# Kernel tuning notes

Hardware: AMD Instinct MI355X
Metric: run time of the kernel (lower is better)

## Reference

```python
import jax, jax.numpy as jnp
import numpy as np

EMB_DIM = 1024
NUM_HEADS = 16
HEAD_DIM = EMB_DIM // NUM_HEADS


def setup_inputs() -> dict:
    key = jax.random.key(0)
    ks = jax.random.split(key, 10)
    B, Sq, Skv = 4, 4096, 4096
    scale = 1.0 / np.sqrt(EMB_DIM)
    inp = {
        "query": jax.random.normal(ks[0], (B, Sq, EMB_DIM), jnp.float32),
        "key_value": jax.random.normal(ks[1], (B, Skv, EMB_DIM), jnp.float32),
        "Wq": jax.random.normal(ks[2], (EMB_DIM, EMB_DIM), jnp.float32) * scale,
        "bq": jnp.zeros((EMB_DIM,), jnp.float32),
        "Wk": jax.random.normal(ks[3], (EMB_DIM, EMB_DIM), jnp.float32) * scale,
        "bk": jnp.zeros((EMB_DIM,), jnp.float32),
        "Wv": jax.random.normal(ks[4], (EMB_DIM, EMB_DIM), jnp.float32) * scale,
        "bv": jnp.zeros((EMB_DIM,), jnp.float32),
        "Wo": jax.random.normal(ks[5], (EMB_DIM, EMB_DIM), jnp.float32) * scale,
        "bo": jnp.zeros((EMB_DIM,), jnp.float32),
    }
    return inp


def reference(query, key_value, Wq, bq, Wk, bk, Wv, bv, Wo, bo):
    B, Sq, D = query.shape
    Skv = key_value.shape[1]
    H, hd = NUM_HEADS, HEAD_DIM
    # Projections -> [B, S, H, hd]
    Q = (query @ Wq + bq).reshape(B, Sq, H, hd)
    K = (key_value @ Wk + bk).reshape(B, Skv, H, hd)
    V = (key_value @ Wv + bv).reshape(B, Skv, H, hd)
    # elu+1 feature map (strictly positive)
    Q = jax.nn.elu(Q) + 1.0
    K = jax.nn.elu(K) + 1.0
    # KV summarization: [B, H, hd, hd]
    KV = jnp.einsum("bshd,bshe->bhde", K, V)
    K_sum = K.sum(axis=1)  # [B, H, hd]
    # Attention output and normalizer
    out = jnp.einsum("bqhd,bhde->bqhe", Q, KV)          # [B, Sq, H, hd]
    norm = jnp.einsum("bqhd,bhd->bqh", Q, K_sum)         # [B, Sq, H]
    out = out / (norm[..., None] + 1e-6)
    out = out.reshape(B, Sq, D)
    return out @ Wo + bo  # dropout is identity in eval
```

## Files before the change

kernel.cpp:

```cpp
#include <hip/hip_runtime.h>

typedef __bf16 bf16_t;
typedef __bf16 bf16x2 __attribute__((ext_vector_type(2)));
typedef __bf16 bf16x8 __attribute__((ext_vector_type(8)));
typedef float floatx4 __attribute__((ext_vector_type(4)));

#define B_ 4
#define S_ 4096
#define D_ 1024
#define H_ 16
#define HD_ 64
#define M_TOT (B_ * S_)

#define BM 128
#define BN 128
#define BK 64

__device__ __forceinline__ void async_load16(const bf16_t* g, bf16_t* l) {
  __builtin_amdgcn_global_load_lds(
      (const __attribute__((address_space(1))) void*)g,
      (__attribute__((address_space(3))) void*)l,
      16, 0, 0);
}

struct PrepArgs {
  const float* q; const float* kv;
  bf16_t* aq; bf16_t* akv;
  const float* w0; const float* w1; const float* w2; const float* w3;
  bf16_t* t0; bf16_t* t1; bf16_t* t2; bf16_t* t3;
  float* zbase;
};

__global__ __launch_bounds__(256) void prep_kernel(PrepArgs p) {
  __shared__ float tile[32][33];
  const int bid = blockIdx.x;
  const int t = threadIdx.x;
  if (bid < 16384) {
    const float* in = bid < 8192 ? p.q : p.kv;
    bf16_t* out = bid < 8192 ? p.aq : p.akv;
    int i = ((bid & 8191) * 256 + t) * 8;
    float4 a = *(const float4*)(in + i);
    float4 b = *(const float4*)(in + i + 4);
    bf16x8 o;
    o[0] = (bf16_t)a.x; o[1] = (bf16_t)a.y; o[2] = (bf16_t)a.z; o[3] = (bf16_t)a.w;
    o[4] = (bf16_t)b.x; o[5] = (bf16_t)b.y; o[6] = (bf16_t)b.z; o[7] = (bf16_t)b.w;
    *(bf16x8*)(out + i) = o;
  } else if (bid < 20480) {
    int idx = bid - 16384;
    int z = idx >> 10;
    int rem = idx & 1023;
    const float* W = z == 0 ? p.w0 : z == 1 ? p.w1 : z == 2 ? p.w2 : p.w3;
    bf16_t* Wt = z == 0 ? p.t0 : z == 1 ? p.t1 : z == 2 ? p.t2 : p.t3;
    int n0 = (rem & 31) * 32;
    int k0 = (rem >> 5) * 32;
    int tx = t & 31;
    int ty = t >> 5;
    for (int r = ty; r < 32; r += 8)
      tile[r][tx] = W[(size_t)(k0 + r) * D_ + n0 + tx];
    __syncthreads();
    for (int r = ty; r < 32; r += 8)
      Wt[(size_t)(n0 + r) * D_ + k0 + tx] = (bf16_t)tile[tx][r];
  } else {
    int idx = bid - 20480;
    ((float4*)p.zbase)[idx * 256 + t] = (float4){0.f, 0.f, 0.f, 0.f};
  }
}

struct ProjArgs {
  const bf16_t* Aq; const bf16_t* Akv;
  const bf16_t* WqT; const bf16_t* WkvT;
  const float* bq; const float* bk; const float* bv;
  bf16_t* Qf; bf16_t* Kf; bf16_t* Vf;
};

__global__ __launch_bounds__(256) void proj_kernel(ProjArgs p) {
  __shared__ __attribute__((aligned(16))) bf16_t As[BM * BK];
  __shared__ __attribute__((aligned(16))) bf16_t Bs[BN * BK];
  const int t = threadIdx.x;
  const int w = t >> 6;
  const int lane = t & 63;

  const unsigned L = blockIdx.x;
  const unsigned xcd = L & 7;
  const unsigned slot = L >> 3;
  const unsigned mt = xcd * 16 + slot / 24u;
  const unsigned nt = slot % 24u;
  const int row0 = mt * BM;
  const bool isQ = nt < 8;
  const bf16_t* A  = isQ ? p.Aq : p.Akv;
  const bf16_t* Bt = isQ ? p.WqT : p.WkvT;
  const int col0 = (isQ ? nt : nt - 8) * BN;

  const int wm = (w & 1) * 64;
  const int wn = (w >> 1) * 64;
  const int lr = lane & 15;
  const int lq = lane >> 4;
  const int rx = lr & 7;

  floatx4 acc[4][4];
#pragma unroll
  for (int i = 0; i < 4; ++i)
#pragma unroll
    for (int j = 0; j < 4; ++j) acc[i][j] = (floatx4){0.f, 0.f, 0.f, 0.f};

  for (int kt = 0; kt < D_; kt += BK) {
#pragma unroll
    for (int j = 0; j < 4; ++j) {
      int s = j * 256 + t;
      int r = s >> 3;
      int cs = (((s & 7) ^ (r & 7)) << 3);
      async_load16(&A[(size_t)(row0 + r) * D_ + kt + cs], &As[j * 2048 + w * 512]);
      async_load16(&Bt[(size_t)(col0 + r) * D_ + kt + cs], &Bs[j * 2048 + w * 512]);
    }
    __syncthreads();
#pragma unroll
    for (int ks = 0; ks < BK; ks += 32) {
      const int go = ((lq + (ks >> 3)) ^ rx) << 3;
      bf16x8 af[4], bfr[4];
#pragma unroll
      for (int i = 0; i < 4; ++i)
        af[i] = *(const bf16x8*)&As[(wm + i * 16 + lr) * BK + go];
#pragma unroll
      for (int j = 0; j < 4; ++j)
        bfr[j] = *(const bf16x8*)&Bs[(wn + j * 16 + lr) * BK + go];
#pragma unroll
      for (int i = 0; i < 4; ++i)
#pragma unroll
        for (int j = 0; j < 4; ++j)
          acc[i][j] = __builtin_amdgcn_mfma_f32_16x16x32_bf16(af[i], bfr[j], acc[i][j], 0, 0, 0);
    }
    __syncthreads();
  }

#pragma unroll
  for (int i = 0; i < 4; ++i) {
#pragma unroll
    for (int j = 0; j < 4; ++j) {
      int gr = row0 + wm + i * 16 + lq * 4;
      int gc = col0 + wn + j * 16 + lr;
      if (isQ) {
        float bsv = p.bq[gc];
#pragma unroll
        for (int r = 0; r < 4; ++r) {
          float v = acc[i][j][r] + bsv;
          v = v > 0.f ? v + 1.f : __expf(v);
          p.Qf[(size_t)(gr + r) * 1024 + gc] = (bf16_t)v;
        }
      } else if (gc < 1024) {
        float bsv = p.bk[gc];
#pragma unroll
        for (int r = 0; r < 4; ++r) {
          float v = acc[i][j][r] + bsv;
          v = v > 0.f ? v + 1.f : __expf(v);
          p.Kf[(size_t)(gr + r) * 1024 + gc] = (bf16_t)v;
        }
      } else {
        float bsv = p.bv[gc - 1024];
#pragma unroll
        for (int r = 0; r < 4; ++r) {
          float v = acc[i][j][r] + bsv;
          p.Vf[(size_t)(gr + r) * 1024 + (gc - 1024)] = (bf16_t)v;
        }
      }
    }
  }
}

__global__ __launch_bounds__(256) void gemm_out_kernel(
    const bf16_t* __restrict__ A,
    const bf16_t* __restrict__ Bt,
    const float* __restrict__ bias,
    float* __restrict__ outf) {
  __shared__ __attribute__((aligned(16))) bf16_t As[BM * BK];
  __shared__ __attribute__((aligned(16))) bf16_t Bs[BN * BK];
  const int t = threadIdx.x;
  const int w = t >> 6;
  const int lane = t & 63;

  const int L = blockIdx.y * gridDim.x + blockIdx.x;
  const int xcd = L & 7;
  const int slot = L >> 3;
  const int mt = xcd * 16 + (slot >> 3);
  const int nt = slot & 7;
  const int row0 = mt * BM;
  const int col0 = nt * BN;

  const int wm = (w & 1) * 64;
  const int wn = (w >> 1) * 64;
  const int lr = lane & 15;
  const int lq = lane >> 4;
  const int rx = lr & 7;

  floatx4 acc[4][4];
#pragma unroll
  for (int i = 0; i < 4; ++i)
#pragma unroll
    for (int j = 0; j < 4; ++j) acc[i][j] = (floatx4){0.f, 0.f, 0.f, 0.f};

  for (int kt = 0; kt < D_; kt += BK) {
#pragma unroll
    for (int j = 0; j < 4; ++j) {
      int s = j * 256 + t;
      int r = s >> 3;
      int cs = (((s & 7) ^ (r & 7)) << 3);
      async_load16(&A[(size_t)(row0 + r) * D_ + kt + cs], &As[j * 2048 + w * 512]);
      async_load16(&Bt[(size_t)(col0 + r) * D_ + kt + cs], &Bs[j * 2048 + w * 512]);
    }
    __syncthreads();
#pragma unroll
    for (int ks = 0; ks < BK; ks += 32) {
      const int go = ((lq + (ks >> 3)) ^ rx) << 3;
      bf16x8 af[4], bfr[4];
#pragma unroll
      for (int i = 0; i < 4; ++i)
        af[i] = *(const bf16x8*)&As[(wm + i * 16 + lr) * BK + go];
#pragma unroll
      for (int j = 0; j < 4; ++j)
        bfr[j] = *(const bf16x8*)&Bs[(wn + j * 16 + lr) * BK + go];
#pragma unroll
      for (int i = 0; i < 4; ++i)
#pragma unroll
        for (int j = 0; j < 4; ++j)
          acc[i][j] = __builtin_amdgcn_mfma_f32_16x16x32_bf16(af[i], bfr[j], acc[i][j], 0, 0, 0);
    }
    __syncthreads();
  }

#pragma unroll
  for (int i = 0; i < 4; ++i) {
#pragma unroll
    for (int j = 0; j < 4; ++j) {
      int gr = row0 + wm + i * 16 + lq * 4;
      int gc = col0 + wn + j * 16 + lr;
      float bsv = bias[gc];
#pragma unroll
      for (int r = 0; r < 4; ++r)
        outf[(size_t)(gr + r) * D_ + gc] = acc[i][j][r] + bsv;
    }
  }
}

#define KVP 68
__global__ __launch_bounds__(256) void kv_mfma_kernel(
    const bf16_t* __restrict__ Kf, const bf16_t* __restrict__ Vf,
    float* __restrict__ KVtg, float* __restrict__ Ksumg) {
  __shared__ __attribute__((aligned(16))) bf16_t Kt[64 * KVP];
  __shared__ __attribute__((aligned(16))) bf16_t Vt[64 * KVP];
  const int t = threadIdx.x;
  const int w = t >> 6, lane = t & 63;
  const int lr = lane & 15, lq = lane >> 4;
  const int bh = blockIdx.x, sc = blockIdx.y;
  const int b = bh >> 4, h = bh & 15;
  const size_t base = (size_t)b * S_ * D_ + (size_t)h * HD_;
  const int p = t >> 3;
  const int c0 = (t & 7) * 8;

  floatx4 acc[4], accn[4];
#pragma unroll
  for (int j = 0; j < 4; ++j) {
    acc[j] = (floatx4){0.f, 0.f, 0.f, 0.f};
    accn[j] = (floatx4){0.f, 0.f, 0.f, 0.f};
  }
  bf16x8 ones;
#pragma unroll
  for (int u = 0; u < 8; ++u) ones[u] = (bf16_t)(lr == 0 ? 1.f : 0.f);

  for (int st = 0; st < 8; ++st) {
    int s0 = sc * 512 + st * 64;
    bf16x8 ka = *(const bf16x8*)&Kf[base + (size_t)(s0 + 2 * p) * D_ + c0];
    bf16x8 kb = *(const bf16x8*)&Kf[base + (size_t)(s0 + 2 * p + 1) * D_ + c0];
    bf16x8 va = *(const bf16x8*)&Vf[base + (size_t)(s0 + 2 * p) * D_ + c0];
    bf16x8 vb = *(const bf16x8*)&Vf[base + (size_t)(s0 + 2 * p + 1) * D_ + c0];
    __syncthreads();
#pragma unroll
    for (int u = 0; u < 8; ++u) {
      *(bf16x2*)&Kt[(c0 + u) * KVP + 2 * p] = (bf16x2){ka[u], kb[u]};
      *(bf16x2*)&Vt[(c0 + u) * KVP + 2 * p] = (bf16x2){va[u], vb[u]};
    }
    __syncthreads();
#pragma unroll
    for (int ks = 0; ks < 2; ++ks) {
      bf16x8 af = *(const bf16x8*)&Vt[(w * 16 + lr) * KVP + ks * 32 + lq * 8];
      bf16x8 bf_[4];
#pragma unroll
      for (int j = 0; j < 4; ++j)
        bf_[j] = *(const bf16x8*)&Kt[(j * 16 + lr) * KVP + ks * 32 + lq * 8];
#pragma unroll
      for (int j = 0; j < 4; ++j)
        acc[j] = __builtin_amdgcn_mfma_f32_16x16x32_bf16(af, bf_[j], acc[j], 0, 0, 0);
      if (w == 0) {
#pragma unroll
        for (int j = 0; j < 4; ++j)
          accn[j] = __builtin_amdgcn_mfma_f32_16x16x32_bf16(ones, bf_[j], accn[j], 0, 0, 0);
      }
    }
  }
  float* kvp = KVtg + (size_t)bh * 4096;
#pragma unroll
  for (int j = 0; j < 4; ++j)
#pragma unroll
    for (int r = 0; r < 4; ++r)
      atomicAdd(&kvp[(w * 16 + lq * 4 + r) * 64 + j * 16 + lr], acc[j][r]);
  if (w == 0 && lq == 0) {
#pragma unroll
    for (int j = 0; j < 4; ++j)
      atomicAdd(&Ksumg[bh * 64 + j * 16 + lr], accn[j][0]);
  }
}

__global__ __launch_bounds__(256) void attend_mfma_kernel(
    const bf16_t* __restrict__ Qf, const float* __restrict__ KVtg,
    const float* __restrict__ Ksumg, bf16_t* __restrict__ X) {
  __shared__ __attribute__((aligned(16))) bf16_t As[256 * 64];
  __shared__ __attribute__((aligned(16))) bf16_t Bs[64 * 64];
  const int t = threadIdx.x;
  const int w = t >> 6;
  const int lane = t & 63;
  const int lr = lane & 15;
  const int lq = lane >> 4;
  const int rx = lr & 7;
  const int bh = blockIdx.y;
  const int b = bh >> 4, h = bh & 15;
  const int q0 = blockIdx.x * 256;
  const size_t qbase = ((size_t)b * S_ + q0) * D_ + (size_t)h * HD_;

  {
    const int r8 = lane >> 3;
    const int cs = (((lane & 7) ^ (r8 & 7)) << 3);
#pragma unroll
    for (int it = 0; it < 8; ++it) {
      int r = w * 64 + it * 8 + r8;
      async_load16(&Qf[qbase + (size_t)r * D_ + cs], &As[(w * 64 + it * 8) * 64]);
    }
  }
  {
    const float* src = KVtg + (size_t)bh * 4096;
    int i0 = t * 16;
    float4 f0 = *(const float4*)(src + i0);
    float4 f1 = *(const float4*)(src + i0 + 4);
    float4 f2 = *(const float4*)(src + i0 + 8);
    float4 f3 = *(const float4*)(src + i0 + 12);
    bf16x8 o1, o2;
    o1[0] = (bf16_t)f0.x; o1[1] = (bf16_t)f0.y; o1[2] = (bf16_t)f0.z; o1[3] = (bf16_t)f0.w;
    o1[4] = (bf16_t)f1.x; o1[5] = (bf16_t)f1.y; o1[6] = (bf16_t)f1.z; o1[7] = (bf16_t)f1.w;
    o2[0] = (bf16_t)f2.x; o2[1] = (bf16_t)f2.y; o2[2] = (bf16_t)f2.z; o2[3] = (bf16_t)f2.w;
    o2[4] = (bf16_t)f3.x; o2[5] = (bf16_t)f3.y; o2[6] = (bf16_t)f3.z; o2[7] = (bf16_t)f3.w;
    int r = t >> 2;
    int cc = (t & 3) * 2;
    int rxw = r & 7;
    *(bf16x8*)&Bs[r * 64 + ((cc ^ rxw) << 3)] = o1;
    *(bf16x8*)&Bs[r * 64 + (((cc + 1) ^ rxw) << 3)] = o2;
  }

  bf16x8 bn[2];
#pragma unroll
  for (int ks = 0; ks < 2; ++ks) {
    bf16x8 z;
#pragma unroll
    for (int u = 0; u < 8; ++u) z[u] = (bf16_t)0.f;
    if (lr == 0) {
      const float* kp = &Ksumg[bh * 64 + ks * 32 + lq * 8];
      float4 k1 = *(const float4*)kp;
      float4 k2 = *(const float4*)(kp + 4);
      z[0] = (bf16_t)k1.x; z[1] = (bf16_t)k1.y; z[2] = (bf16_t)k1.z; z[3] = (bf16_t)k1.w;
      z[4] = (bf16_t)k2.x; z[5] = (bf16_t)k2.y; z[6] = (bf16_t)k2.z; z[7] = (bf16_t)k2.w;
    }
    bn[ks] = z;
  }

  floatx4 acc[4][4];
  floatx4 accn[4];
#pragma unroll
  for (int i = 0; i < 4; ++i) {
    accn[i] = (floatx4){0.f, 0.f, 0.f, 0.f};
#pragma unroll
    for (int j = 0; j < 4; ++j) acc[i][j] = (floatx4){0.f, 0.f, 0.f, 0.f};
  }

  __syncthreads();

#pragma unroll
  for (int ks = 0; ks < 2; ++ks) {
    const int go = ((lq + ks * 4) ^ rx) << 3;
    bf16x8 af[4], bfr[4];
#pragma unroll
    for (int i = 0; i < 4; ++i)
      af[i] = *(const bf16x8*)&As[(w * 64 + i * 16 + lr) * 64 + go];
#pragma unroll
    for (int j = 0; j < 4; ++j)
      bfr[j] = *(const bf16x8*)&Bs[(j * 16 + lr) * 64 + go];
#pragma unroll
    for (int i = 0; i < 4; ++i) {
#pragma unroll
      for (int j = 0; j < 4; ++j)
        acc[i][j] = __builtin_amdgcn_mfma_f32_16x16x32_bf16(af[i], bfr[j], acc[i][j], 0, 0, 0);
      accn[i] = __builtin_amdgcn_mfma_f32_16x16x32_bf16(af[i], bn[ks], accn[i], 0, 0, 0);
    }
  }

#pragma unroll
  for (int i = 0; i < 4; ++i) {
    int rowb = q0 + w * 64 + i * 16 + lq * 4;
#pragma unroll
    for (int r = 0; r < 4; ++r) {
      float nr = __shfl(accn[i][r], lane & 48);
      float inv = 1.f / (nr + 1e-6f);
      size_t rb = ((size_t)b * S_ + rowb + r) * D_ + (size_t)h * HD_;
#pragma unroll
      for (int j = 0; j < 4; ++j)
        X[rb + j * 16 + lr] = (bf16_t)(acc[i][j][r] * inv);
    }
  }
}

extern "C" void kernel_launch(void* const* d_in, const int* in_sizes, int n_in,
                              void* d_out, int out_size, void* d_ws, size_t ws_size,
                              hipStream_t stream) {
  const float* query     = (const float*)d_in[0];
  const float* key_value = (const float*)d_in[1];
  const float* Wq = (const float*)d_in[2];
  const float* bq = (const float*)d_in[3];
  const float* Wk = (const float*)d_in[4];
  const float* bk = (const float*)d_in[5];
  const float* Wv = (const float*)d_in[6];
  const float* bv = (const float*)d_in[7];
  const float* Wo = (const float*)d_in[8];
  const float* bo = (const float*)d_in[9];
  float* out = (float*)d_out;

  char* ws = (char*)d_ws;
  const size_t MB = 1024 * 1024;
  bf16_t* Aq   = (bf16_t*)(ws + 0);
  bf16_t* Akv  = (bf16_t*)(ws + 32 * MB);
  bf16_t* WqT  = (bf16_t*)(ws + 64 * MB);
  bf16_t* WkT  = (bf16_t*)(ws + 66 * MB);
  bf16_t* WvT  = (bf16_t*)(ws + 68 * MB);
  bf16_t* WoT  = (bf16_t*)(ws + 70 * MB);
  bf16_t* Qf   = (bf16_t*)(ws + 72 * MB);
  bf16_t* Kf   = (bf16_t*)(ws + 104 * MB);
  bf16_t* Vf   = (bf16_t*)(ws + 136 * MB);
  float*  KVtg = (float*)(ws + 168 * MB);
  float*  Ksumg= (float*)(ws + 169 * MB);

  PrepArgs pa = {query, key_value, Aq, Akv, Wq, Wk, Wv, Wo, WqT, WkT, WvT, WoT, KVtg};
  prep_kernel<<<20740, 256, 0, stream>>>(pa);

  ProjArgs pj = {Aq, Akv, WqT, WkT, bq, bk, bv, Qf, Kf, Vf};
  proj_kernel<<<3072, 256, 0, stream>>>(pj);

  dim3 kvgrid(64, 8);
  kv_mfma_kernel<<<kvgrid, 256, 0, stream>>>(Kf, Vf, KVtg, Ksumg);

  dim3 agrid(S_ / 256, 64);
  attend_mfma_kernel<<<agrid, 256, 0, stream>>>(Qf, KVtg, Ksumg, Aq );

  dim3 ggrid(D_ / BN, M_TOT / BM);
  gemm_out_kernel<<<ggrid, 256, 0, stream>>>(Aq, WoT, bo, out);
}
```

Measured before the change: 409.1 us.

## Use 256x256 pipelined GEMM tiles and replace KV atomics with partial-sum reduction

```diff
diff --git a/kernel.cpp b/kernel.cpp
--- a/kernel.cpp
+++ b/kernel.cpp
@@ -12,10 +12,6 @@
 #define HD_ 64
 #define M_TOT (B_ * S_)
 
-#define BM 128
-#define BN 128
-#define BK 64
-
 __device__ __forceinline__ void async_load16(const bf16_t* g, bf16_t* l) {
   __builtin_amdgcn_global_load_lds(
       (const __attribute__((address_space(1))) void*)g,
@@ -28,7 +24,6 @@
   bf16_t* aq; bf16_t* akv;
   const float* w0; const float* w1; const float* w2; const float* w3;
   bf16_t* t0; bf16_t* t1; bf16_t* t2; bf16_t* t3;
-  float* zbase;
 };
 
 __global__ __launch_bounds__(256) void prep_kernel(PrepArgs p) {
@@ -45,7 +40,7 @@
     o[0] = (bf16_t)a.x; o[1] = (bf16_t)a.y; o[2] = (bf16_t)a.z; o[3] = (bf16_t)a.w;
     o[4] = (bf16_t)b.x; o[5] = (bf16_t)b.y; o[6] = (bf16_t)b.z; o[7] = (bf16_t)b.w;
     *(bf16x8*)(out + i) = o;
-  } else if (bid < 20480) {
+  } else {
     int idx = bid - 16384;
     int z = idx >> 10;
     int rem = idx & 1023;
@@ -60,10 +55,73 @@
     __syncthreads();
     for (int r = ty; r < 32; r += 8)
       Wt[(size_t)(n0 + r) * D_ + k0 + tx] = (bf16_t)tile[tx][r];
-  } else {
-    int idx = bid - 20480;
-    ((float4*)p.zbase)[idx * 256 + t] = (float4){0.f, 0.f, 0.f, 0.f};
-  }
+  }
+}
+
+__device__ __forceinline__ void gemm256_core(
+    const bf16_t* __restrict__ A, const bf16_t* __restrict__ Bt,
+    int row0, int col0, bf16_t* As, bf16_t* Bs, floatx4 (&acc)[8][4]) {
+  const int tid = threadIdx.x;
+  const int w = tid >> 6;
+  const int lane = tid & 63;
+  const int lr = lane & 15;
+  const int lq = lane >> 4;
+  const int wm0 = (w >> 2) * 128;
+  const int wn0 = (w & 3) * 64;
+
+  const int c0 = w * 64 + lane;
+  const int c1 = c0 + 512;
+  const int r0 = c0 >> 2, q0 = c0 & 3;
+  const int r1 = c1 >> 2, q1 = c1 & 3;
+  const size_t offA0 = (size_t)(row0 + r0) * D_ + ((q0 ^ ((r0 >> 1) & 3)) * 8);
+  const size_t offA1 = (size_t)(row0 + r1) * D_ + ((q1 ^ ((r1 >> 1) & 3)) * 8);
+  const size_t offB0 = (size_t)(col0 + r0) * D_ + ((q0 ^ ((r0 >> 1) & 3)) * 8);
+  const size_t offB1 = (size_t)(col0 + r1) * D_ + ((q1 ^ ((r1 >> 1) & 3)) * 8);
+  const int ldst0 = w * 512;
+  const int ldst1 = 4096 + w * 512;
+  const int swz = (lq ^ ((lr >> 1) & 3)) * 8;
+
+#define STAGE_TILE(tt)                                   \
+  {                                                      \
+    bf16_t* as_ = As + ((tt) & 3) * 8192;                \
+    bf16_t* bs_ = Bs + ((tt) & 3) * 8192;                \
+    const int ko_ = (tt) * 32;                           \
+    async_load16(A + offA0 + ko_, as_ + ldst0);          \
+    async_load16(A + offA1 + ko_, as_ + ldst1);          \
+    async_load16(Bt + offB0 + ko_, bs_ + ldst0);         \
+    async_load16(Bt + offB1 + ko_, bs_ + ldst1);         \
+  }
+
+  STAGE_TILE(0)
+  STAGE_TILE(1)
+
+  for (int kt = 0; kt < 32; ++kt) {
+    if (kt < 30) {
+      STAGE_TILE(kt + 2)
+      asm volatile("s_waitcnt vmcnt(8)\n\ts_barrier" ::: "memory");
+    } else if (kt == 30) {
+      asm volatile("s_waitcnt vmcnt(4)\n\ts_barrier" ::: "memory");
+    } else {
+      asm volatile("s_waitcnt vmcnt(0)\n\ts_barrier" ::: "memory");
+    }
+    const bf16_t* as = As + (kt & 3) * 8192;
+    const bf16_t* bs = Bs + (kt & 3) * 8192;
+    bf16x8 af[8], bfr[4];
+#pragma unroll
+    for (int i = 0; i < 8; ++i)
+      af[i] = *(const bf16x8*)&as[(wm0 + i * 16 + lr) * 32 + swz];
+#pragma unroll
+    for (int j = 0; j < 4; ++j)
+      bfr[j] = *(const bf16x8*)&bs[(wn0 + j * 16 + lr) * 32 + swz];
+    __builtin_amdgcn_s_setprio(1);
+#pragma unroll
+    for (int i = 0; i < 8; ++i)
+#pragma unroll
+      for (int j = 0; j < 4; ++j)
+        acc[i][j] = __builtin_amdgcn_mfma_f32_16x16x32_bf16(af[i], bfr[j], acc[i][j], 0, 0, 0);
+    __builtin_amdgcn_s_setprio(0);
+  }
+#undef STAGE_TILE
 }
 
 struct ProjArgs {
@@ -73,165 +131,128 @@
   bf16_t* Qf; bf16_t* Kf; bf16_t* Vf;
 };
 
-__global__ __launch_bounds__(256) void proj_kernel(ProjArgs p) {
-  __shared__ __attribute__((aligned(16))) bf16_t As[BM * BK];
-  __shared__ __attribute__((aligned(16))) bf16_t Bs[BN * BK];
-  const int t = threadIdx.x;
-  const int w = t >> 6;
-  const int lane = t & 63;
-
+__global__ __launch_bounds__(512, 2) void proj256_kernel(ProjArgs p) {
+  __shared__ __attribute__((aligned(16))) bf16_t As[4 * 8192];
+  __shared__ __attribute__((aligned(16))) bf16_t Bs[4 * 8192];
   const unsigned L = blockIdx.x;
   const unsigned xcd = L & 7;
   const unsigned slot = L >> 3;
-  const unsigned mt = xcd * 16 + slot / 24u;
-  const unsigned nt = slot % 24u;
-  const int row0 = mt * BM;
-  const bool isQ = nt < 8;
-  const bf16_t* A  = isQ ? p.Aq : p.Akv;
+  const unsigned mq = slot / 24u;
+  const unsigned s24 = slot % 24u;
+  const int mt = xcd * 8 + mq * 2 + (s24 & 1);
+  const int nt = s24 >> 1;
+  const bool isQ = nt < 4;
+  const int row0 = mt * 256;
+  const int col0 = (isQ ? nt : nt - 4) * 256;
+  const bf16_t* A = isQ ? p.Aq : p.Akv;
   const bf16_t* Bt = isQ ? p.WqT : p.WkvT;
-  const int col0 = (isQ ? nt : nt - 8) * BN;
-
-  const int wm = (w & 1) * 64;
-  const int wn = (w >> 1) * 64;
+
+  floatx4 acc[8][4];
+#pragma unroll
+  for (int i = 0; i < 8; ++i)
+#pragma unroll
+    for (int j = 0; j < 4; ++j) acc[i][j] = (floatx4){0.f, 0.f, 0.f, 0.f};
+
+  gemm256_core(A, Bt, row0, col0, As, Bs, acc);
+
+  const int tid = threadIdx.x;
+  const int w = tid >> 6;
+  const int lane = tid & 63;
   const int lr = lane & 15;
   const int lq = lane >> 4;
-  const int rx = lr & 7;
-
-  floatx4 acc[4][4];
-#pragma unroll
-  for (int i = 0; i < 4; ++i)
-#pragma unroll
-    for (int j = 0; j < 4; ++j) acc[i][j] = (floatx4){0.f, 0.f, 0.f, 0.f};
-
-  for (int kt = 0; kt < D_; kt += BK) {
-#pragma unroll
-    for (int j = 0; j < 4; ++j) {
-      int s = j * 256 + t;
-      int r = s >> 3;
-      int cs = (((s & 7) ^ (r & 7)) << 3);
-      async_load16(&A[(size_t)(row0 + r) * D_ + kt + cs], &As[j * 2048 + w * 512]);
-      async_load16(&Bt[(size_t)(col0 + r) * D_ + kt + cs], &Bs[j * 2048 + w * 512]);
-    }
-    __syncthreads();
-#pragma unroll
-    for (int ks = 0; ks < BK; ks += 32) {
-      const int go = ((lq + (ks >> 3)) ^ rx) << 3;
-      bf16x8 af[4], bfr[4];
-#pragma unroll
-      for (int i = 0; i < 4; ++i)
-        af[i] = *(const bf16x8*)&As[(wm + i * 16 + lr) * BK + go];
-#pragma unroll
-      for (int j = 0; j < 4; ++j)
-        bfr[j] = *(const bf16x8*)&Bs[(wn + j * 16 + lr) * BK + go];
-#pragma unroll
-      for (int i = 0; i < 4; ++i)
-#pragma unroll
-        for (int j = 0; j < 4; ++j)
-          acc[i][j] = __builtin_amdgcn_mfma_f32_16x16x32_bf16(af[i], bfr[j], acc[i][j], 0, 0, 0);
-    }
-    __syncthreads();
-  }
-
-#pragma unroll
-  for (int i = 0; i < 4; ++i) {
-#pragma unroll
-    for (int j = 0; j < 4; ++j) {
-      int gr = row0 + wm + i * 16 + lq * 4;
-      int gc = col0 + wn + j * 16 + lr;
-      if (isQ) {
+  const int wm0 = (w >> 2) * 128;
+  const int wn0 = (w & 3) * 64;
+
+  if (isQ) {
+#pragma unroll
+    for (int i = 0; i < 8; ++i) {
+      int gr = row0 + wm0 + i * 16 + lq * 4;
+#pragma unroll
+      for (int j = 0; j < 4; ++j) {
+        int gc = col0 + wn0 + j * 16 + lr;
         float bsv = p.bq[gc];
 #pragma unroll
         for (int r = 0; r < 4; ++r) {
           float v = acc[i][j][r] + bsv;
           v = v > 0.f ? v + 1.f : __expf(v);
-          p.Qf[(size_t)(gr + r) * 1024 + gc] = (bf16_t)v;
+          p.Qf[(size_t)(gr + r) * D_ + gc] = (bf16_t)v;
         }
-      } else if (gc < 1024) {
+      }
+    }
+  } else if (nt < 8) {
+#pragma unroll
+    for (int i = 0; i < 8; ++i) {
+      int gr = row0 + wm0 + i * 16 + lq * 4;
+#pragma unroll
+      for (int j = 0; j < 4; ++j) {
+        int gc = col0 + wn0 + j * 16 + lr;
         float bsv = p.bk[gc];
 #pragma unroll
         for (int r = 0; r < 4; ++r) {
           float v = acc[i][j][r] + bsv;
           v = v > 0.f ? v + 1.f : __expf(v);
-          p.Kf[(size_t)(gr + r) * 1024 + gc] = (bf16_t)v;
+          p.Kf[(size_t)(gr + r) * D_ + gc] = (bf16_t)v;
         }
-      } else {
-        float bsv = p.bv[gc - 1024];
+      }
+    }
+  } else {
+#pragma unroll
+    for (int i = 0; i < 8; ++i) {
+      int gr = row0 + wm0 + i * 16 + lq * 4;
+#pragma unroll
+      for (int j = 0; j < 4; ++j) {
+        int gc = col0 + wn0 + j * 16 + lr;
+        int vc = gc - 1024;
+        float bsv = p.bv[vc];
 #pragma unroll
         for (int r = 0; r < 4; ++r) {
           float v = acc[i][j][r] + bsv;
-          p.Vf[(size_t)(gr + r) * 1024 + (gc - 1024)] = (bf16_t)v;
+          p.Vf[(size_t)(gr + r) * D_ + vc] = (bf16_t)v;
         }
       }
     }
   }
 }
 
-__global__ __launch_bounds__(256) void gemm_out_kernel(
+__global__ __launch_bounds__(512, 2) void gemm_out256_kernel(
     const bf16_t* __restrict__ A,
     const bf16_t* __restrict__ Bt,
     const float* __restrict__ bias,
     float* __restrict__ outf) {
-  __shared__ __attribute__((aligned(16))) bf16_t As[BM * BK];
-  __shared__ __attribute__((aligned(16))) bf16_t Bs[BN * BK];
-  const int t = threadIdx.x;
-  const int w = t >> 6;
-  const int lane = t & 63;
-
-  const int L = blockIdx.y * gridDim.x + blockIdx.x;
-  const int xcd = L & 7;
-  const int slot = L >> 3;
-  const int mt = xcd * 16 + (slot >> 3);
-  const int nt = slot & 7;
-  const int row0 = mt * BM;
-  const int col0 = nt * BN;
-
-  const int wm = (w & 1) * 64;
-  const int wn = (w >> 1) * 64;
+  __shared__ __attribute__((aligned(16))) bf16_t As[4 * 8192];
+  __shared__ __attribute__((aligned(16))) bf16_t Bs[4 * 8192];
+  const unsigned L = blockIdx.x;
+  const unsigned xcd = L & 7;
+  const unsigned slot = L >> 3;
+  const unsigned mq = slot >> 3;
+  const unsigned s8 = slot & 7;
+  const int mt = xcd * 8 + mq * 2 + (s8 & 1);
+  const int nt = s8 >> 1;
+  const int row0 = mt * 256;
+  const int col0 = nt * 256;
+
+  floatx4 acc[8][4];
+#pragma unroll
+  for (int i = 0; i < 8; ++i)
+#pragma unroll
+    for (int j = 0; j < 4; ++j) acc[i][j] = (floatx4){0.f, 0.f, 0.f, 0.f};
+
+  gemm256_core(A, Bt, row0, col0, As, Bs, acc);
+
+  const int tid = threadIdx.x;
+  const int w = tid >> 6;
+  const int lane = tid & 63;
   const int lr = lane & 15;
   const int lq = lane >> 4;
-  const int rx = lr & 7;
-
-  floatx4 acc[4][4];
-#pragma unroll
-  for (int i = 0; i < 4; ++i)
-#pragma unroll
-    for (int j = 0; j < 4; ++j) acc[i][j] = (floatx4){0.f, 0.f, 0.f, 0.f};
-
-  for (int kt = 0; kt < D_; kt += BK) {
+  const int wm0 = (w >> 2) * 128;
+  const int wn0 = (w & 3) * 64;
+
+#pragma unroll
+  for (int i = 0; i < 8; ++i) {
+    int gr = row0 + wm0 + i * 16 + lq * 4;
 #pragma unroll
     for (int j = 0; j < 4; ++j) {
-      int s = j * 256 + t;
-      int r = s >> 3;
-      int cs = (((s & 7) ^ (r & 7)) << 3);
-      async_load16(&A[(size_t)(row0 + r) * D_ + kt + cs], &As[j * 2048 + w * 512]);
-      async_load16(&Bt[(size_t)(col0 + r) * D_ + kt + cs], &Bs[j * 2048 + w * 512]);
-    }
-    __syncthreads();
-#pragma unroll
-    for (int ks = 0; ks < BK; ks += 32) {
-      const int go = ((lq + (ks >> 3)) ^ rx) << 3;
-      bf16x8 af[4], bfr[4];
-#pragma unroll
-      for (int i = 0; i < 4; ++i)
-        af[i] = *(const bf16x8*)&As[(wm + i * 16 + lr) * BK + go];
-#pragma unroll
-      for (int j = 0; j < 4; ++j)
-        bfr[j] = *(const bf16x8*)&Bs[(wn + j * 16 + lr) * BK + go];
-#pragma unroll
-      for (int i = 0; i < 4; ++i)
-#pragma unroll
-        for (int j = 0; j < 4; ++j)
-          acc[i][j] = __builtin_amdgcn_mfma_f32_16x16x32_bf16(af[i], bfr[j], acc[i][j], 0, 0, 0);
-    }
-    __syncthreads();
-  }
-
-#pragma unroll
-  for (int i = 0; i < 4; ++i) {
-#pragma unroll
-    for (int j = 0; j < 4; ++j) {
-      int gr = row0 + wm + i * 16 + lq * 4;
-      int gc = col0 + wn + j * 16 + lr;
+      int gc = col0 + wn0 + j * 16 + lr;
       float bsv = bias[gc];
 #pragma unroll
       for (int r = 0; r < 4; ++r)
@@ -243,7 +264,7 @@
 #define KVP 68
 __global__ __launch_bounds__(256) void kv_mfma_kernel(
     const bf16_t* __restrict__ Kf, const bf16_t* __restrict__ Vf,
-    float* __restrict__ KVtg, float* __restrict__ Ksumg) {
+    float* __restrict__ KVpart, float* __restrict__ Kspart) {
   __shared__ __attribute__((aligned(16))) bf16_t Kt[64 * KVP];
   __shared__ __attribute__((aligned(16))) bf16_t Vt[64 * KVP];
   const int t = threadIdx.x;
@@ -295,16 +316,46 @@
       }
     }
   }
-  float* kvp = KVtg + (size_t)bh * 4096;
+  float* kvp = KVpart + ((size_t)bh * 8 + sc) * 4096;
 #pragma unroll
   for (int j = 0; j < 4; ++j)
 #pragma unroll
     for (int r = 0; r < 4; ++r)
-      atomicAdd(&kvp[(w * 16 + lq * 4 + r) * 64 + j * 16 + lr], acc[j][r]);
+      kvp[(w * 16 + lq * 4 + r) * 64 + j * 16 + lr] = acc[j][r];
   if (w == 0 && lq == 0) {
 #pragma unroll
     for (int j = 0; j < 4; ++j)
-      atomicAdd(&Ksumg[bh * 64 + j * 16 + lr], accn[j][0]);
+      Kspart[((size_t)bh * 8 + sc) * 64 + j * 16 + lr] = accn[j][0];
+  }
+}
+
+__global__ __launch_bounds__(256) void kv_reduce_kernel(
+    const float* __restrict__ KVpart, const float* __restrict__ Kspart,
+    float* __restrict__ KVtg, float* __restrict__ Ksumg) {
+  const int bid = blockIdx.x;
+  const int t = threadIdx.x;
+  if (bid < 256) {
+    int idx4 = bid * 256 + t;
+    int bh = idx4 >> 10;
+    int d4 = idx4 & 1023;
+    float4 s = {0.f, 0.f, 0.f, 0.f};
+#pragma unroll
+    for (int sc = 0; sc < 8; ++sc) {
+      float4 v = *(const float4*)&KVpart[((size_t)bh * 8 + sc) * 4096 + d4 * 4];
+      s.x += v.x; s.y += v.y; s.z += v.z; s.w += v.w;
+    }
+    *(float4*)&KVtg[(size_t)bh * 4096 + d4 * 4] = s;
+  } else {
+    int idx = (bid - 256) * 256 + t;
+    int bh = idx >> 4;
+    int d4 = idx & 15;
+    float4 s = {0.f, 0.f, 0.f, 0.f};
+#pragma unroll
+    for (int sc = 0; sc < 8; ++sc) {
+      float4 v = *(const float4*)&Kspart[((size_t)bh * 8 + sc) * 64 + d4 * 4];
+      s.x += v.x; s.y += v.y; s.z += v.z; s.w += v.w;
+    }
+    *(float4*)&Ksumg[bh * 64 + d4 * 4] = s;
   }
 }
 
@@ -432,6 +483,8 @@
   const size_t MB = 1024 * 1024;
   bf16_t* Aq   = (bf16_t*)(ws + 0);
   bf16_t* Akv  = (bf16_t*)(ws + 32 * MB);
+  float*  KVpart = (float*)(ws + 32 * MB);
+  float*  Kspart = (float*)(ws + 40 * MB);
   bf16_t* WqT  = (bf16_t*)(ws + 64 * MB);
   bf16_t* WkT  = (bf16_t*)(ws + 66 * MB);
   bf16_t* WvT  = (bf16_t*)(ws + 68 * MB);
@@ -442,18 +495,19 @@
   float*  KVtg = (float*)(ws + 168 * MB);
   float*  Ksumg= (float*)(ws + 169 * MB);
 
-  PrepArgs pa = {query, key_value, Aq, Akv, Wq, Wk, Wv, Wo, WqT, WkT, WvT, WoT, KVtg};
-  prep_kernel<<<20740, 256, 0, stream>>>(pa);
+  PrepArgs pa = {query, key_value, Aq, Akv, Wq, Wk, Wv, Wo, WqT, WkT, WvT, WoT};
+  prep_kernel<<<20480, 256, 0, stream>>>(pa);
 
   ProjArgs pj = {Aq, Akv, WqT, WkT, bq, bk, bv, Qf, Kf, Vf};
-  proj_kernel<<<3072, 256, 0, stream>>>(pj);
+  proj256_kernel<<<768, 512, 0, stream>>>(pj);
 
   dim3 kvgrid(64, 8);
-  kv_mfma_kernel<<<kvgrid, 256, 0, stream>>>(Kf, Vf, KVtg, Ksumg);
+  kv_mfma_kernel<<<kvgrid, 256, 0, stream>>>(Kf, Vf, KVpart, Kspart);
+
+  kv_reduce_kernel<<<260, 256, 0, stream>>>(KVpart, Kspart, KVtg, Ksumg);
 
   dim3 agrid(S_ / 256, 64);
   attend_mfma_kernel<<<agrid, 256, 0, stream>>>(Qf, KVtg, Ksumg, Aq );
 
-  dim3 ggrid(D_ / BN, M_TOT / BM);
-  gemm_out_kernel<<<ggrid, 256, 0, stream>>>(Aq, WoT, bo, out);
-}
+  gemm_out256_kernel<<<256, 512, 0, stream>>>(Aq, WoT, bo, out);
+}
```

New measurement: 367.1 us. 10.3% less time.
